# Kernel optimization log

Measured on AMD Instinct MI355X. Metric: run time of the kernel, lower is better.

## Reference

```python
import jax, jax.numpy as jnp
import numpy as np

B, C, D, H, W = 4, 256, 16, 16, 16
INTER = C // 8  # 32


def setup_inputs() -> dict:
    key = jax.random.key(0)
    ks = jax.random.split(key, 8)
    return {
        "x": jax.random.normal(ks[0], (B, C, D, H, W), dtype=jnp.float32),
        "Wq": jax.random.normal(ks[1], (INTER, C), dtype=jnp.float32) * 0.05,
        "bq": jax.random.normal(ks[2], (INTER,), dtype=jnp.float32) * 0.05,
        "Wk": jax.random.normal(ks[3], (INTER, C), dtype=jnp.float32) * 0.05,
        "bk": jax.random.normal(ks[4], (INTER,), dtype=jnp.float32) * 0.05,
        "Wv": jax.random.normal(ks[5], (C, C), dtype=jnp.float32) * 0.05,
        "bv": jax.random.normal(ks[6], (C,), dtype=jnp.float32) * 0.05,
        "gamma": jax.random.normal(ks[7], (1,), dtype=jnp.float32),
    }


def reference(x, Wq, bq, Wk, bk, Wv, bv, gamma):
    b, c, d, h, w = x.shape
    n = d * h * w
    xf = x.reshape(b, c, n)  # [B, C, N]
    # 1x1 Conv3d == pointwise channel projection
    q = jnp.einsum("oc,bcn->bon", Wq, xf) + bq[None, :, None]  # [B, inter, N]
    k = jnp.einsum("oc,bcn->bon", Wk, xf) + bk[None, :, None]  # [B, inter, N]
    v = jnp.einsum("oc,bcn->bon", Wv, xf) + bv[None, :, None]  # [B, C, N]
    scale = float(q.shape[1]) ** 0.5
    # attn[b, i, j] = <q[:, i], k[:, j]>
    attn = jax.nn.softmax(jnp.einsum("bci,bcj->bij", q, k) / scale, axis=-1)
    # out[b, c, i] = sum_j v[b, c, j] * attn[b, i, j]
    out = jnp.einsum("bcj,bij->bci", v, attn).reshape(b, c, d, h, w)
    return gamma[0] * out + x
```

## Files before the change

### kernel.cpp

```cpp
#include <hip/hip_runtime.h>

#define B_ 4
#define C_ 256
#define N_ 4096
#define INTER_ 32

typedef __attribute__((ext_vector_type(8))) short short8;
typedef __attribute__((ext_vector_type(4))) float f32x4;
typedef __attribute__((ext_vector_type(16))) float f32x16;
typedef __attribute__((ext_vector_type(4))) unsigned int u32x4;

#define TILEB 18432
#define NSTG  (4 * TILEB)

static __device__ __forceinline__ unsigned short f2bf(float f) {
    unsigned int u = __builtin_bit_cast(unsigned int, f);
    u += 0x7fff + ((u >> 16) & 1);
    return (unsigned short)(u >> 16);
}

static __device__ __forceinline__ unsigned int cvtpk(float lo, float hi) {
    unsigned int r;
    asm("v_cvt_pk_bf16_f32 %0, %1, %2" : "=v"(r) : "v"(lo), "v"(hi));
    return r;
}

static __device__ __forceinline__ void pl32swap(unsigned int& a, unsigned int& b) {
    asm("v_permlane32_swap_b32 %0, %1" : "+v"(a), "+v"(b));
}

static __device__ __forceinline__ float exp2a(float x) {
    float r;
    asm("v_exp_f32 %0, %1" : "=v"(r) : "v"(x));
    return r;
}

static __device__ __forceinline__ void gload16(const void* g, void* l) {
    __builtin_amdgcn_global_load_lds(
        (const __attribute__((address_space(1))) void*)g,
        (__attribute__((address_space(3))) void*)l, 16, 0, 0);
}

__global__ __launch_bounds__(256) void prep_kernel(
    const float* __restrict__ Wq, const float* __restrict__ Wk,
    const float* __restrict__ Wv, unsigned short* __restrict__ wb)
{
    int i = blockIdx.x * 256 + threadIdx.x;
    int row = i >> 8, col = i & 255;
    float v;
    if (row < 32)      v = Wq[row * 256 + col];
    else if (row < 64) v = Wk[(row - 32) * 256 + col];
    else               v = Wv[(row - 64) * 256 + col];
    wb[i] = f2bf(v);
}

__global__ __launch_bounds__(256) void qkv_kernel(
    const float* __restrict__ x, const unsigned short* __restrict__ wb,
    const float* __restrict__ bq, const float* __restrict__ bk,
    const float* __restrict__ bv,
    unsigned short* __restrict__ qb, unsigned short* __restrict__ kfrag,
    unsigned short* __restrict__ vfrag)
{
    const int tid  = threadIdx.x;
    const int wave = tid >> 6;
    const int lane = tid & 63;
    const int l31  = lane & 31;
    const int h2   = lane >> 5;
    const int b    = blockIdx.x >> 6;
    const int n0   = (blockIdx.x & 63) * 64;

    __shared__ unsigned int xsh[64 * 129];

    {
        const float* xb = x + ((size_t)b * C_ + 64 * wave) * N_ + n0 + lane;
        unsigned int* dst = xsh + (size_t)lane * 129 + 32 * wave;
        #pragma unroll 8
        for (int s = 0; s < 32; ++s) {
            float v0 = xb[(size_t)(2 * s) * N_];
            float v1 = xb[(size_t)(2 * s + 1) * N_];
            dst[s] = (unsigned int)f2bf(v0) | ((unsigned int)f2bf(v1) << 16);
        }
    }
    __syncthreads();

    const float rs = 0.25504183f;

    #pragma unroll
    for (int u = 0; u < 5; ++u) {
        const int unit = wave + 4 * u;
        const int ch = unit >> 1;
        const int ns = unit & 1;
        const int ncol = n0 + 32 * ns + l31;
        const int jt = (n0 >> 5) + ns;

        const float* bias = (ch == 0) ? bq : (ch == 1) ? bk : (bv + (ch - 2) * 32);
        f32x16 acc;
        #pragma unroll
        for (int r = 0; r < 16; ++r)
            acc[r] = bias[(r & 3) + 8 * (r >> 2) + 4 * h2];

        const unsigned short* wrow = wb + ((size_t)(ch * 32 + l31)) * 256 + 8 * h2;
        const unsigned int*   xrow = xsh + (size_t)(32 * ns + l31) * 129 + 4 * h2;

        #pragma unroll
        for (int kk = 0; kk < 16; ++kk) {
            short8 wa = *reinterpret_cast<const short8*>(wrow + 16 * kk);
            short8 xf = *reinterpret_cast<const short8*>(xrow + 8 * kk);
            acc = __builtin_amdgcn_mfma_f32_32x32x16_bf16(wa, xf, acc, 0, 0, 0);
        }

        if (ch == 0) {
            unsigned short* dst = qb + ((size_t)b * N_ + ncol) * 32;
            #pragma unroll
            for (int q = 0; q < 4; ++q) {
                unsigned int w0 = (unsigned int)f2bf(acc[4 * q] * rs)
                                | ((unsigned int)f2bf(acc[4 * q + 1] * rs) << 16);
                unsigned int w1 = (unsigned int)f2bf(acc[4 * q + 2] * rs)
                                | ((unsigned int)f2bf(acc[4 * q + 3] * rs) << 16);
                unsigned int* p = reinterpret_cast<unsigned int*>(dst + 4 * h2 + 8 * q);
                p[0] = w0; p[1] = w1;
            }
        } else if (ch == 1) {
            unsigned short* kt = kfrag + ((size_t)b * 128 + jt) * 1024;
            #pragma unroll
            for (int r = 0; r < 16; ++r) {
                const int co = (r & 3) + 8 * (r >> 2) + 4 * h2;
                const int addr = ((co >> 4) << 9) + ((l31 + 32 * ((co >> 3) & 1)) << 3)
                               + (co & 7);
                kt[addr] = f2bf(acc[r]);
            }
        } else {
            const int g = ch - 2;
            unsigned short* vt_ = vfrag + (((size_t)b * 128 + jt) * 8 + g) * 1024;
            #pragma unroll
            for (int r = 0; r < 16; ++r) {
                const int co = (r & 3) + 8 * (r >> 2) + 4 * h2;
                const int addr = ((l31 >> 4) << 9) + ((co + 32 * ((l31 >> 3) & 1)) << 3)
                               + (l31 & 7);
                vt_[addr] = f2bf(acc[r]);
            }
        }
    }
}

__global__ __launch_bounds__(256, 2) void attn_kernel(
    const unsigned short* __restrict__ qb, const unsigned short* __restrict__ kfrag,
    const unsigned short* __restrict__ vfrag,
    const float* __restrict__ x, const float* __restrict__ gamma,
    float* __restrict__ out)
{
    const int tid  = threadIdx.x;
    const int wave = tid >> 6;
    const int lane = tid & 63;
    const int l31  = lane & 31;
    const int h2   = lane >> 5;
    const int jq   = wave >> 1;
    const int qs   = wave & 1;

    const int bid  = blockIdx.x;
    const int xcd  = bid & 7;
    const int slot = bid >> 3;
    const int b    = xcd >> 1;
    const int ib   = slot * 2 + (xcd & 1);
    const int iq   = ib * 64 + 32 * qs;

    __shared__ char lds[NSTG];
    __shared__ float m_sh[4][32];
    __shared__ float l_sh[4][32];

    const unsigned short* vtb = vfrag + (size_t)b * 128 * 8192;
    const unsigned short* ktb = kfrag + (size_t)b * 128 * 1024;

    char* reg0 = lds + (jq * 2) * TILEB;
    char* reg1 = reg0 + TILEB;

    short8 qf0 = *reinterpret_cast<const short8*>(
        qb + ((size_t)b * N_ + iq + l31) * 32 + 8 * h2);
    short8 qf1 = *reinterpret_cast<const short8*>(
        qb + ((size_t)b * N_ + iq + l31) * 32 + 8 * h2 + 16);

    f32x16 acc[8];
    #pragma unroll
    for (int g = 0; g < 8; ++g)
        #pragma unroll
        for (int r = 0; r < 16; ++r) acc[g][r] = 0.f;

    float m_run = 0.f;
    float l_run = 0.f;
    const f32x16 z16 = {};

    {
        const char* vs = (const char*)(vtb + (size_t)(jq * 64) * 8192);
        const char* ks = (const char*)(ktb + (size_t)(jq * 64) * 1024);
        #pragma unroll
        for (int s2 = 0; s2 < 9; ++s2) {
            const int off = qs * 9216 + s2 * 1024;
            const char* g = (off < 16384) ? (vs + off) : (ks + (off - 16384));
            gload16(g + lane * 16, reg0 + off);
        }
    }
    __syncthreads();

    #pragma unroll 1
    for (int t = 0; t < 64; ++t) {
        char* cur = (t & 1) ? reg1 : reg0;
        char* nxt = (t & 1) ? reg0 : reg1;

        if (t < 63) {
            const int jtg = jq * 64 + t + 1;
            const char* vs = (const char*)(vtb + (size_t)jtg * 8192);
            const char* ks = (const char*)(ktb + (size_t)jtg * 1024);
            #pragma unroll
            for (int s2 = 0; s2 < 9; ++s2) {
                const int off = qs * 9216 + s2 * 1024;
                const char* g = (off < 16384) ? (vs + off) : (ks + (off - 16384));
                gload16(g + lane * 16, nxt + off);
            }
        }

        const char* kt_ = cur + 16384;
        short8 ka0 = *reinterpret_cast<const short8*>(kt_ + lane * 16);
        short8 ka1 = *reinterpret_cast<const short8*>(kt_ + 1024 + lane * 16);
        f32x16 s = __builtin_amdgcn_mfma_f32_32x32x16_bf16(ka0, qf0, z16, 0, 0, 0);
        s = __builtin_amdgcn_mfma_f32_32x32x16_bf16(ka1, qf1, s, 0, 0, 0);

        float a0 = fmaxf(s[0], s[8]),  a1 = fmaxf(s[1], s[9]);
        float a2 = fmaxf(s[2], s[10]), a3 = fmaxf(s[3], s[11]);
        float a4 = fmaxf(s[4], s[12]), a5 = fmaxf(s[5], s[13]);
        float a6 = fmaxf(s[6], s[14]), a7 = fmaxf(s[7], s[15]);
        a0 = fmaxf(a0, a4); a1 = fmaxf(a1, a5); a2 = fmaxf(a2, a6); a3 = fmaxf(a3, a7);
        float smax = fmaxf(fmaxf(a0, a1), fmaxf(a2, a3));

        if (__any(smax > m_run + 8.0f)) {
            float sm2 = fmaxf(smax, __shfl_xor(smax, 32));
            float mnew = fmaxf(m_run, sm2);
            float corr = exp2a(m_run - mnew);
            m_run = mnew;
            l_run *= corr;
            #pragma unroll
            for (int g = 0; g < 8; ++g)
                #pragma unroll
                for (int r = 0; r < 16; ++r) acc[g][r] *= corr;
        }

        float p[16];
        float lsum = 0.f;
        #pragma unroll
        for (int r = 0; r < 16; ++r) { p[r] = exp2a(s[r] - m_run); lsum += p[r]; }
        l_run += lsum;

        unsigned int X0 = cvtpk(p[0],  p[1]),  X1 = cvtpk(p[2],  p[3]);
        unsigned int Y0 = cvtpk(p[4],  p[5]),  Y1 = cvtpk(p[6],  p[7]);
        unsigned int W0 = cvtpk(p[8],  p[9]),  W1 = cvtpk(p[10], p[11]);
        unsigned int V0 = cvtpk(p[12], p[13]), V1 = cvtpk(p[14], p[15]);
        pl32swap(X0, Y0); pl32swap(X1, Y1);
        pl32swap(W0, V0); pl32swap(W1, V1);
        short8 pb0 = __builtin_bit_cast(short8, u32x4{X0, X1, Y0, Y1});
        short8 pb1 = __builtin_bit_cast(short8, u32x4{W0, W1, V0, V1});

        __builtin_amdgcn_s_setprio(1);
        #pragma unroll
        for (int g = 0; g < 8; ++g) {
            short8 va0 = *reinterpret_cast<const short8*>(cur + g * 2048 + lane * 16);
            short8 va1 = *reinterpret_cast<const short8*>(cur + g * 2048 + 1024 + lane * 16);
            acc[g] = __builtin_amdgcn_mfma_f32_32x32x16_bf16(va0, pb0, acc[g], 0, 0, 0);
            acc[g] = __builtin_amdgcn_mfma_f32_32x32x16_bf16(va1, pb1, acc[g], 0, 0, 0);
        }
        __builtin_amdgcn_s_setprio(0);

        __syncthreads();
    }

    float l_tot = l_run + __shfl_xor(l_run, 32);
    if (lane < 32) { m_sh[wave][lane] = m_run; l_sh[wave][lane] = l_tot; }
    __syncthreads();

    const float m0 = m_sh[qs][l31];
    const float m1 = m_sh[2 + qs][l31];
    const float M  = fmaxf(m0, m1);
    const float L  = exp2a(m0 - M) * l_sh[qs][l31]
                   + exp2a(m1 - M) * l_sh[2 + qs][l31];
    const float wgt = exp2a(m_run - M);
    #pragma unroll
    for (int g = 0; g < 8; ++g)
        #pragma unroll
        for (int r = 0; r < 16; ++r) acc[g][r] *= wgt;

    f32x4* D = reinterpret_cast<f32x4*>(lds);
    if (jq == 1) {
        #pragma unroll
        for (int g = 0; g < 8; ++g)
            #pragma unroll
            for (int r4 = 0; r4 < 4; ++r4) {
                f32x4 tv;
                #pragma unroll
                for (int e = 0; e < 4; ++e) tv[e] = acc[g][4 * r4 + e];
                D[qs * 2048 + (g * 4 + r4) * 64 + lane] = tv;
            }
    }
    __syncthreads();
    if (jq == 0) {
        #pragma unroll
        for (int g = 0; g < 8; ++g)
            #pragma unroll
            for (int r4 = 0; r4 < 4; ++r4) {
                f32x4 tv = D[qs * 2048 + (g * 4 + r4) * 64 + lane];
                #pragma unroll
                for (int e = 0; e < 4; ++e) tv[e] += acc[g][4 * r4 + e];
                D[qs * 2048 + (g * 4 + r4) * 64 + lane] = tv;
            }
    }
    __syncthreads();

    const float gma  = gamma[0];
    const float invL = 1.f / L;
    const int i = iq + l31;
    #pragma unroll
    for (int gi = 0; gi < 4; ++gi) {
        const int g = jq * 4 + gi;
        #pragma unroll
        for (int r4 = 0; r4 < 4; ++r4) {
            f32x4 v = D[qs * 2048 + (g * 4 + r4) * 64 + lane];
            #pragma unroll
            for (int e = 0; e < 4; ++e) {
                const int c = 32 * g + e + 8 * r4 + 4 * h2;
                const size_t off = ((size_t)b * C_ + c) * N_ + i;
                out[off] = gma * v[e] * invL + x[off];
            }
        }
    }
}

extern "C" void kernel_launch(void* const* d_in, const int* in_sizes, int n_in,
                              void* d_out, int out_size, void* d_ws, size_t ws_size,
                              hipStream_t stream) {
    const float* x     = (const float*)d_in[0];
    const float* Wq    = (const float*)d_in[1];
    const float* bq    = (const float*)d_in[2];
    const float* Wk    = (const float*)d_in[3];
    const float* bk    = (const float*)d_in[4];
    const float* Wv    = (const float*)d_in[5];
    const float* bv    = (const float*)d_in[6];
    const float* gamma = (const float*)d_in[7];
    float* out = (float*)d_out;

    unsigned short* ws = (unsigned short*)d_ws;
    unsigned short* qb    = ws;
    unsigned short* kfrag = qb + (size_t)B_ * N_ * INTER_;
    unsigned short* vfrag = kfrag + (size_t)B_ * 128 * 1024;
    unsigned short* wb    = vfrag + (size_t)B_ * 128 * 8192;

    prep_kernel<<<dim3(320), 256, 0, stream>>>(Wq, Wk, Wv, wb);
    qkv_kernel<<<dim3(B_ * (N_ / 64)), 256, 0, stream>>>(
        x, wb, bq, bk, bv, qb, kfrag, vfrag);
    attn_kernel<<<dim3(256), 256, 0, stream>>>(
        qb, kfrag, vfrag, x, gamma, out);
}
```

Baseline: 93.77 us.

## Split attention into producer waves for softmax and consumer waves for PV MFMA

Restructures the attention kernel into 512-thread blocks. Four producer waves compute QK scores, the online softmax and bf16 P tiles, and write P plus rescale flags and factors to LDS. Four consumer waves run the PV MFMAs against a triple-buffered V tile in LDS, lagging one step behind. The aim is to overlap the exp/softmax work with the V matmul and to share V loads across both query row groups. In exchange it uses about 122 KB of LDS per block, adds an LDS round trip for P, and adds rescale-flag traffic.

```diff
diff --git a/kernel.cpp b/kernel.cpp
--- a/kernel.cpp
+++ b/kernel.cpp
@@ -10,8 +10,12 @@
 typedef __attribute__((ext_vector_type(16))) float f32x16;
 typedef __attribute__((ext_vector_type(4))) unsigned int u32x4;
 
-#define TILEB 18432
-#define NSTG  (4 * TILEB)
+#define VOFF  0
+#define KOFF  98304
+#define POFF  106496
+#define FOFF  122880
+#define MOFF  124160
+#define LDSSZ 125184
 
 static __device__ __forceinline__ unsigned short f2bf(float f) {
     unsigned int u = __builtin_bit_cast(unsigned int, f);
@@ -143,7 +147,7 @@
     }
 }
 
-__global__ __launch_bounds__(256, 2) void attn_kernel(
+__global__ __launch_bounds__(512, 2) void attn_kernel(
     const unsigned short* __restrict__ qb, const unsigned short* __restrict__ kfrag,
     const unsigned short* __restrict__ vfrag,
     const float* __restrict__ x, const float* __restrict__ gamma,
@@ -154,173 +158,231 @@
     const int lane = tid & 63;
     const int l31  = lane & 31;
     const int h2   = lane >> 5;
-    const int jq   = wave >> 1;
-    const int qs   = wave & 1;
+    const bool prod = wave < 4;
+    const int jq = wave & 1;
+    const int rg = wave >> 1;
+    const int ch = (wave - 4) >> 1;
 
     const int bid  = blockIdx.x;
     const int xcd  = bid & 7;
     const int slot = bid >> 3;
     const int b    = xcd >> 1;
     const int ib   = slot * 2 + (xcd & 1);
-    const int iq   = ib * 64 + 32 * qs;
-
-    __shared__ char lds[NSTG];
-    __shared__ float m_sh[4][32];
-    __shared__ float l_sh[4][32];
+    const int i0   = ib * 64;
+
+    __shared__ char lds[LDSSZ];
 
     const unsigned short* vtb = vfrag + (size_t)b * 128 * 8192;
     const unsigned short* ktb = kfrag + (size_t)b * 128 * 1024;
 
-    char* reg0 = lds + (jq * 2) * TILEB;
-    char* reg1 = reg0 + TILEB;
-
-    short8 qf0 = *reinterpret_cast<const short8*>(
-        qb + ((size_t)b * N_ + iq + l31) * 32 + 8 * h2);
-    short8 qf1 = *reinterpret_cast<const short8*>(
-        qb + ((size_t)b * N_ + iq + l31) * 32 + 8 * h2 + 16);
-
-    f32x16 acc[8];
+    char* ldsV = lds + VOFF + jq * 49152;
+    char* ldsK = lds + KOFF + jq * 4096;
+    const int jt0 = jq * 64;
+
+    short8 qf0{}, qf1{};
+    float m_run = 0.f, l_run = 0.f;
+    if (prod) {
+        const unsigned short* qbase =
+            qb + ((size_t)b * N_ + i0 + rg * 32 + l31) * 32 + 8 * h2;
+        qf0 = *reinterpret_cast<const short8*>(qbase);
+        qf1 = *reinterpret_cast<const short8*>(qbase + 16);
+    }
+    f32x16 acc[2][4];
     #pragma unroll
-    for (int g = 0; g < 8; ++g)
-        #pragma unroll
-        for (int r = 0; r < 16; ++r) acc[g][r] = 0.f;
-
-    float m_run = 0.f;
-    float l_run = 0.f;
+    for (int a = 0; a < 2; ++a)
+        #pragma unroll
+        for (int g = 0; g < 4; ++g)
+            #pragma unroll
+            for (int r = 0; r < 16; ++r) acc[a][g][r] = 0.f;
+
     const f32x16 z16 = {};
 
-    {
-        const char* vs = (const char*)(vtb + (size_t)(jq * 64) * 8192);
-        const char* ks = (const char*)(ktb + (size_t)(jq * 64) * 1024);
-        #pragma unroll
-        for (int s2 = 0; s2 < 9; ++s2) {
-            const int off = qs * 9216 + s2 * 1024;
-            const char* g = (off < 16384) ? (vs + off) : (ks + (off - 16384));
-            gload16(g + lane * 16, reg0 + off);
-        }
-    }
+#define PROD_STEP(T) do {                                                     \
+        const int kb_ = (T) & 1;                                              \
+        const char* kc = ldsK + kb_ * 2048;                                   \
+        short8 ka0 = *reinterpret_cast<const short8*>(kc + lane * 16);        \
+        short8 ka1 = *reinterpret_cast<const short8*>(kc + 1024 + lane * 16); \
+        f32x16 s = __builtin_amdgcn_mfma_f32_32x32x16_bf16(ka0, qf0, z16, 0, 0, 0); \
+        s = __builtin_amdgcn_mfma_f32_32x32x16_bf16(ka1, qf1, s, 0, 0, 0);    \
+        float a0 = fmaxf(s[0], s[8]),  a1 = fmaxf(s[1], s[9]);                \
+        float a2 = fmaxf(s[2], s[10]), a3 = fmaxf(s[3], s[11]);               \
+        float a4 = fmaxf(s[4], s[12]), a5 = fmaxf(s[5], s[13]);               \
+        float a6 = fmaxf(s[6], s[14]), a7 = fmaxf(s[7], s[15]);               \
+        a0 = fmaxf(a0, a4); a1 = fmaxf(a1, a5);                               \
+        a2 = fmaxf(a2, a6); a3 = fmaxf(a3, a7);                               \
+        float smax = fmaxf(fmaxf(a0, a1), fmaxf(a2, a3));                     \
+        const int resc_i = __any(smax > m_run + 8.0f);                        \
+        char* Fw = lds + FOFF + ((jq * 2 + kb_) * 2 + rg) * 160;              \
+        if (resc_i) {                                                         \
+            float sm2 = fmaxf(smax, __shfl_xor(smax, 32));                    \
+            float mnew = fmaxf(m_run, sm2);                                   \
+            float corr = exp2a(m_run - mnew);                                 \
+            m_run = mnew; l_run *= corr;                                      \
+            if (lane < 32) *reinterpret_cast<float*>(Fw + 16 + l31 * 4) = corr; \
+        }                                                                     \
+        if (lane == 0) *reinterpret_cast<int*>(Fw) = resc_i;                  \
+        float p_[16]; float lsum = 0.f;                                       \
+        _Pragma("unroll")                                                     \
+        for (int r = 0; r < 16; ++r) { p_[r] = exp2a(s[r] - m_run); lsum += p_[r]; } \
+        l_run += lsum;                                                        \
+        unsigned int X0 = cvtpk(p_[0],  p_[1]),  X1 = cvtpk(p_[2],  p_[3]);   \
+        unsigned int Y0 = cvtpk(p_[4],  p_[5]),  Y1 = cvtpk(p_[6],  p_[7]);   \
+        unsigned int W0 = cvtpk(p_[8],  p_[9]),  W1 = cvtpk(p_[10], p_[11]);  \
+        unsigned int V0 = cvtpk(p_[12], p_[13]), V1 = cvtpk(p_[14], p_[15]);  \
+        pl32swap(X0, Y0); pl32swap(X1, Y1);                                   \
+        pl32swap(W0, V0); pl32swap(W1, V1);                                   \
+        char* Pw = lds + POFF + ((jq * 2 + kb_) * 2 + rg) * 2048;             \
+        *reinterpret_cast<u32x4*>(Pw + lane * 16) = u32x4{X0, X1, Y0, Y1};    \
+        *reinterpret_cast<u32x4*>(Pw + 1024 + lane * 16) = u32x4{W0, W1, V0, V1}; \
+    } while (0)
+
+#define CONS_STEP(TP) do {                                                    \
+        const int pb_ = (TP) & 1;                                             \
+        const int vs_ = (TP) % 3;                                             \
+        const char* Pr0 = lds + POFF + ((jq * 2 + pb_) * 2 + 0) * 2048;       \
+        const char* Pr1 = lds + POFF + ((jq * 2 + pb_) * 2 + 1) * 2048;       \
+        short8 p00 = *reinterpret_cast<const short8*>(Pr0 + lane * 16);       \
+        short8 p01 = *reinterpret_cast<const short8*>(Pr0 + 1024 + lane * 16);\
+        short8 p10 = *reinterpret_cast<const short8*>(Pr1 + lane * 16);       \
+        short8 p11 = *reinterpret_cast<const short8*>(Pr1 + 1024 + lane * 16);\
+        const char* F0 = lds + FOFF + ((jq * 2 + pb_) * 2 + 0) * 160;         \
+        const char* F1 = lds + FOFF + ((jq * 2 + pb_) * 2 + 1) * 160;         \
+        const int f0 = *reinterpret_cast<const int*>(F0);                     \
+        const int f1 = *reinterpret_cast<const int*>(F1);                     \
+        if (f0) { float c0 = *reinterpret_cast<const float*>(F0 + 16 + l31 * 4); \
+            _Pragma("unroll")                                                 \
+            for (int g = 0; g < 4; ++g)                                       \
+                _Pragma("unroll")                                             \
+                for (int r = 0; r < 16; ++r) acc[0][g][r] *= c0; }            \
+        if (f1) { float c1 = *reinterpret_cast<const float*>(F1 + 16 + l31 * 4); \
+            _Pragma("unroll")                                                 \
+            for (int g = 0; g < 4; ++g)                                       \
+                _Pragma("unroll")                                             \
+                for (int r = 0; r < 16; ++r) acc[1][g][r] *= c1; }            \
+        const char* vb_ = ldsV + vs_ * 16384;                                 \
+        __builtin_amdgcn_s_setprio(1);                                        \
+        _Pragma("unroll")                                                     \
+        for (int gl = 0; gl < 4; ++gl) {                                      \
+            const char* vrow = vb_ + (ch * 4 + gl) * 2048;                    \
+            short8 va0 = *reinterpret_cast<const short8*>(vrow + lane * 16);  \
+            short8 va1 = *reinterpret_cast<const short8*>(vrow + 1024 + lane * 16); \
+            acc[0][gl] = __builtin_amdgcn_mfma_f32_32x32x16_bf16(va0, p00, acc[0][gl], 0, 0, 0); \
+            acc[0][gl] = __builtin_amdgcn_mfma_f32_32x32x16_bf16(va1, p01, acc[0][gl], 0, 0, 0); \
+            acc[1][gl] = __builtin_amdgcn_mfma_f32_32x32x16_bf16(va0, p10, acc[1][gl], 0, 0, 0); \
+            acc[1][gl] = __builtin_amdgcn_mfma_f32_32x32x16_bf16(va1, p11, acc[1][gl], 0, 0, 0); \
+        }                                                                     \
+        __builtin_amdgcn_s_setprio(0);                                        \
+    } while (0)
+
+#define STAGE_K(T) do {                                                       \
+        const char* ks = (const char*)(ktb + (size_t)(jt0 + (T)) * 1024);     \
+        gload16(ks + rg * 1024 + lane * 16,                                   \
+                ldsK + ((T) & 1) * 2048 + rg * 1024);                         \
+    } while (0)
+
+#define STAGE_V(T) do {                                                       \
+        const char* vs = (const char*)(vtb + (size_t)(jt0 + (T)) * 8192);     \
+        char* vw = ldsV + ((T) % 3) * 16384;                                  \
+        _Pragma("unroll")                                                     \
+        for (int s2 = 0; s2 < 8; ++s2)                                        \
+            gload16(vs + (ch * 8 + s2) * 1024 + lane * 16,                    \
+                    vw + (ch * 8 + s2) * 1024);                               \
+    } while (0)
+
+    if (prod) STAGE_K(0); else STAGE_V(0);
+    __syncthreads();
+    if (prod) { STAGE_K(1); PROD_STEP(0); } else { STAGE_V(1); }
     __syncthreads();
 
     #pragma unroll 1
-    for (int t = 0; t < 64; ++t) {
-        char* cur = (t & 1) ? reg1 : reg0;
-        char* nxt = (t & 1) ? reg0 : reg1;
-
-        if (t < 63) {
-            const int jtg = jq * 64 + t + 1;
-            const char* vs = (const char*)(vtb + (size_t)jtg * 8192);
-            const char* ks = (const char*)(ktb + (size_t)jtg * 1024);
-            #pragma unroll
-            for (int s2 = 0; s2 < 9; ++s2) {
-                const int off = qs * 9216 + s2 * 1024;
-                const char* g = (off < 16384) ? (vs + off) : (ks + (off - 16384));
-                gload16(g + lane * 16, nxt + off);
-            }
-        }
-
-        const char* kt_ = cur + 16384;
-        short8 ka0 = *reinterpret_cast<const short8*>(kt_ + lane * 16);
-        short8 ka1 = *reinterpret_cast<const short8*>(kt_ + 1024 + lane * 16);
-        f32x16 s = __builtin_amdgcn_mfma_f32_32x32x16_bf16(ka0, qf0, z16, 0, 0, 0);
-        s = __builtin_amdgcn_mfma_f32_32x32x16_bf16(ka1, qf1, s, 0, 0, 0);
-
-        float a0 = fmaxf(s[0], s[8]),  a1 = fmaxf(s[1], s[9]);
-        float a2 = fmaxf(s[2], s[10]), a3 = fmaxf(s[3], s[11]);
-        float a4 = fmaxf(s[4], s[12]), a5 = fmaxf(s[5], s[13]);
-        float a6 = fmaxf(s[6], s[14]), a7 = fmaxf(s[7], s[15]);
-        a0 = fmaxf(a0, a4); a1 = fmaxf(a1, a5); a2 = fmaxf(a2, a6); a3 = fmaxf(a3, a7);
-        float smax = fmaxf(fmaxf(a0, a1), fmaxf(a2, a3));
-
-        if (__any(smax > m_run + 8.0f)) {
-            float sm2 = fmaxf(smax, __shfl_xor(smax, 32));
-            float mnew = fmaxf(m_run, sm2);
-            float corr = exp2a(m_run - mnew);
-            m_run = mnew;
-            l_run *= corr;
-            #pragma unroll
-            for (int g = 0; g < 8; ++g)
+    for (int t = 1; t < 64; ++t) {
+        if (prod) {
+            if (t < 63) STAGE_K(t + 1);
+            PROD_STEP(t);
+        } else {
+            if (t < 63) STAGE_V(t + 1);
+            CONS_STEP(t - 1);
+        }
+        __syncthreads();
+    }
+    if (!prod) CONS_STEP(63);
+    __syncthreads();
+
+#undef PROD_STEP
+#undef CONS_STEP
+#undef STAGE_K
+#undef STAGE_V
+
+    if (prod && lane < 32) {
+        float l_tot = l_run + __shfl_xor(l_run, 32);
+        *reinterpret_cast<float*>(lds + MOFF + wave * 128 + l31 * 4) = m_run;
+        *reinterpret_cast<float*>(lds + MOFF + 512 + wave * 128 + l31 * 4) = l_tot;
+    }
+    __syncthreads();
+
+#define MSH(pw) (*reinterpret_cast<const float*>(lds + MOFF + (pw) * 128 + l31 * 4))
+#define LSH(pw) (*reinterpret_cast<const float*>(lds + MOFF + 512 + (pw) * 128 + l31 * 4))
+
+    if (!prod) {
+        #pragma unroll
+        for (int rgg = 0; rgg < 2; ++rgg) {
+            const float m0 = MSH(rgg * 2 + 0), m1 = MSH(rgg * 2 + 1);
+            const float M = fmaxf(m0, m1);
+            const float wgt = exp2a(MSH(rgg * 2 + jq) - M);
+            #pragma unroll
+            for (int g = 0; g < 4; ++g)
                 #pragma unroll
-                for (int r = 0; r < 16; ++r) acc[g][r] *= corr;
-        }
-
-        float p[16];
-        float lsum = 0.f;
-        #pragma unroll
-        for (int r = 0; r < 16; ++r) { p[r] = exp2a(s[r] - m_run); lsum += p[r]; }
-        l_run += lsum;
-
-        unsigned int X0 = cvtpk(p[0],  p[1]),  X1 = cvtpk(p[2],  p[3]);
-        unsigned int Y0 = cvtpk(p[4],  p[5]),  Y1 = cvtpk(p[6],  p[7]);
-        unsigned int W0 = cvtpk(p[8],  p[9]),  W1 = cvtpk(p[10], p[11]);
-        unsigned int V0 = cvtpk(p[12], p[13]), V1 = cvtpk(p[14], p[15]);
-        pl32swap(X0, Y0); pl32swap(X1, Y1);
-        pl32swap(W0, V0); pl32swap(W1, V1);
-        short8 pb0 = __builtin_bit_cast(short8, u32x4{X0, X1, Y0, Y1});
-        short8 pb1 = __builtin_bit_cast(short8, u32x4{W0, W1, V0, V1});
-
-        __builtin_amdgcn_s_setprio(1);
-        #pragma unroll
-        for (int g = 0; g < 8; ++g) {
-            short8 va0 = *reinterpret_cast<const short8*>(cur + g * 2048 + lane * 16);
-            short8 va1 = *reinterpret_cast<const short8*>(cur + g * 2048 + 1024 + lane * 16);
-            acc[g] = __builtin_amdgcn_mfma_f32_32x32x16_bf16(va0, pb0, acc[g], 0, 0, 0);
-            acc[g] = __builtin_amdgcn_mfma_f32_32x32x16_bf16(va1, pb1, acc[g], 0, 0, 0);
-        }
-        __builtin_amdgcn_s_setprio(0);
-
-        __syncthreads();
-    }
-
-    float l_tot = l_run + __shfl_xor(l_run, 32);
-    if (lane < 32) { m_sh[wave][lane] = m_run; l_sh[wave][lane] = l_tot; }
-    __syncthreads();
-
-    const float m0 = m_sh[qs][l31];
-    const float m1 = m_sh[2 + qs][l31];
-    const float M  = fmaxf(m0, m1);
-    const float L  = exp2a(m0 - M) * l_sh[qs][l31]
-                   + exp2a(m1 - M) * l_sh[2 + qs][l31];
-    const float wgt = exp2a(m_run - M);
+                for (int r = 0; r < 16; ++r) acc[rgg][g][r] *= wgt;
+        }
+    }
+    if (!prod && jq == 1) {
+        #pragma unroll
+        for (int rgg = 0; rgg < 2; ++rgg)
+            #pragma unroll
+            for (int gl = 0; gl < 4; ++gl)
+                #pragma unroll
+                for (int r4 = 0; r4 < 4; ++r4) {
+                    f32x4 tv;
+                    #pragma unroll
+                    for (int e = 0; e < 4; ++e) tv[e] = acc[rgg][gl][4 * r4 + e];
+                    *reinterpret_cast<f32x4*>(lds +
+                        ((((ch * 2 + rgg) * 4 + gl) * 4 + r4) * 64 + lane) * 16) = tv;
+                }
+    }
+    __syncthreads();
+    if (!prod && jq == 0) {
+        #pragma unroll
+        for (int rgg = 0; rgg < 2; ++rgg)
+            #pragma unroll
+            for (int gl = 0; gl < 4; ++gl)
+                #pragma unroll
+                for (int r4 = 0; r4 < 4; ++r4) {
+                    f32x4* pD = reinterpret_cast<f32x4*>(lds +
+                        ((((ch * 2 + rgg) * 4 + gl) * 4 + r4) * 64 + lane) * 16);
+                    f32x4 tv = *pD;
+                    #pragma unroll
+                    for (int e = 0; e < 4; ++e) tv[e] += acc[rgg][gl][4 * r4 + e];
+                    *pD = tv;
+                }
+    }
+    __syncthreads();
+
+    const float gma = gamma[0];
     #pragma unroll
-    for (int g = 0; g < 8; ++g)
-        #pragma unroll
-        for (int r = 0; r < 16; ++r) acc[g][r] *= wgt;
-
-    f32x4* D = reinterpret_cast<f32x4*>(lds);
-    if (jq == 1) {
-        #pragma unroll
-        for (int g = 0; g < 8; ++g)
-            #pragma unroll
-            for (int r4 = 0; r4 < 4; ++r4) {
-                f32x4 tv;
-                #pragma unroll
-                for (int e = 0; e < 4; ++e) tv[e] = acc[g][4 * r4 + e];
-                D[qs * 2048 + (g * 4 + r4) * 64 + lane] = tv;
-            }
-    }
-    __syncthreads();
-    if (jq == 0) {
-        #pragma unroll
-        for (int g = 0; g < 8; ++g)
-            #pragma unroll
-            for (int r4 = 0; r4 < 4; ++r4) {
-                f32x4 tv = D[qs * 2048 + (g * 4 + r4) * 64 + lane];
-                #pragma unroll
-                for (int e = 0; e < 4; ++e) tv[e] += acc[g][4 * r4 + e];
-                D[qs * 2048 + (g * 4 + r4) * 64 + lane] = tv;
-            }
-    }
-    __syncthreads();
-
-    const float gma  = gamma[0];
-    const float invL = 1.f / L;
-    const int i = iq + l31;
-    #pragma unroll
-    for (int gi = 0; gi < 4; ++gi) {
-        const int g = jq * 4 + gi;
+    for (int k = 0; k < 2; ++k) {
+        const int idx = wave * 2 + k;
+        const int chh = idx >> 3, rgg = (idx >> 2) & 1, gl = idx & 3;
+        const int g = chh * 4 + gl;
+        const float m0 = MSH(rgg * 2 + 0), m1 = MSH(rgg * 2 + 1);
+        const float M = fmaxf(m0, m1);
+        const float L = exp2a(m0 - M) * LSH(rgg * 2 + 0)
+                      + exp2a(m1 - M) * LSH(rgg * 2 + 1);
+        const float invL = 1.f / L;
+        const int i = i0 + rgg * 32 + l31;
         #pragma unroll
         for (int r4 = 0; r4 < 4; ++r4) {
-            f32x4 v = D[qs * 2048 + (g * 4 + r4) * 64 + lane];
+            f32x4 v = *reinterpret_cast<const f32x4*>(lds +
+                ((((chh * 2 + rgg) * 4 + gl) * 4 + r4) * 64 + lane) * 16);
             #pragma unroll
             for (int e = 0; e < 4; ++e) {
                 const int c = 32 * g + e + 8 * r4 + 4 * h2;
@@ -329,6 +391,8 @@
             }
         }
     }
+#undef MSH
+#undef LSH
 }
 
 extern "C" void kernel_launch(void* const* d_in, const int* in_sizes, int n_in,
@@ -353,6 +417,6 @@
     prep_kernel<<<dim3(320), 256, 0, stream>>>(Wq, Wk, Wv, wb);
     qkv_kernel<<<dim3(B_ * (N_ / 64)), 256, 0, stream>>>(
         x, wb, bq, bk, bv, qb, kfrag, vfrag);
-    attn_kernel<<<dim3(256), 256, 0, stream>>>(
+    attn_kernel<<<dim3(256), 512, 0, stream>>>(
         qb, kfrag, vfrag, x, gamma, out);
 }
```

Result: no change. 95.07 us (+1.4%).
